# Kernel tuning notes

Hardware: AMD Instinct MI355X
Metric: run time of the kernel (lower is better)

Reference implementation:

```python
import jax, jax.numpy as jnp
import numpy as np

T, D, E, K = 16384, 2048, 64, 2
LOAD_BALANCE_SCALE = 0.01
NOISY_STD = 1.0


def setup_inputs() -> dict:
    key = jax.random.key(0)
    k1, k2, k3, k4 = jax.random.split(key, 4)
    x_flat = jax.random.normal(k1, (T, D), dtype=jnp.float32)
    noise = jax.random.normal(k2, (T, E), dtype=jnp.float32)
    # gate_linear: nn.Linear(D, E, bias=False) -> weight [E, D]
    W_gate = jax.random.normal(k3, (E, D), dtype=jnp.float32) * (1.0 / np.sqrt(D))
    # noise_weight initialized to zeros in torch; use small values so the
    # noisy path is exercised numerically.
    noise_weight = jax.random.normal(k4, (E,), dtype=jnp.float32) * 0.01
    return {"x_flat": x_flat, "noise": noise, "W_gate": W_gate,
            "noise_weight": noise_weight, "k": K}


def reference(x_flat, noise, W_gate, noise_weight, k):
    # logits = x @ W^T   [T, E]
    logits = jnp.einsum("td,ed->te", x_flat, W_gate)
    logits_noisy = logits + (noise * NOISY_STD) * noise_weight

    # noisy top-k; softmax over -inf-sparse logits == softmax over the k
    # selected logits scattered into zeros (top-k ids are unique per row).
    top_vals, top_ids = jax.lax.top_k(logits_noisy, k)          # [T, k]
    gates_k = jax.nn.softmax(top_vals, axis=-1)                 # [T, k]
    rows = jnp.arange(x_flat.shape[0])[:, None]
    top_k_gated_weights = jnp.zeros_like(logits_noisy).at[rows, top_ids].set(gates_k)

    # load-balance loss on clean logits
    gate_weights_mean = jax.nn.softmax(logits, axis=-1).mean(axis=0)  # [E]
    uniform = jnp.full_like(gate_weights_mean, 1.0 / gate_weights_mean.shape[0])
    load_balance_loss = jnp.mean((gate_weights_mean - uniform) ** 2) * LOAD_BALANCE_SCALE

    return top_k_gated_weights, top_ids, load_balance_loss
```

## Files before the change

### kernel.cpp

```cpp
#include <hip/hip_runtime.h>
#include <hip/hip_bf16.h>

#define T_TOK 16384
#define D_DIM 2048
#define E_EXP 64
#define TAU   2e-3f

typedef __bf16 bf16x8 __attribute__((ext_vector_type(8)));
typedef float  f32x16 __attribute__((ext_vector_type(16)));
typedef unsigned short ushort_t;

#define WS_WHI  0
#define WS_WLO  (256*1024)
#define WS_SUM  (512*1024)
#define WS_CNT  (512*1024 + 512)
#define WS_FLG  (512*1024 + 1024)

__device__ __forceinline__ unsigned short bf16_rne(float x){
  unsigned int u = __float_as_uint(x);
  return (unsigned short)((u + 0x7FFFu + ((u >> 16) & 1u)) >> 16);
}

__device__ __forceinline__ void ins3(float& v1, int& i1, float& v2, int& i2,
                                     float& v3, int& i3, float v, int i){
  if (v > v1 || (v == v1 && i < i1)) { v3=v2; i3=i2; v2=v1; i2=i1; v1=v; i1=i; }
  else if (v > v2 || (v == v2 && i < i2)) { v3=v2; i3=i2; v2=v; i2=i; }
  else if (v > v3 || (v == v3 && i < i3)) { v3=v; i3=i; }
}

__device__ __forceinline__ void gload16(const void* g, const void* l){
  __builtin_amdgcn_global_load_lds(
      (const __attribute__((address_space(1))) unsigned int*)g,
      (__attribute__((address_space(3))) unsigned int*)l, 16, 0, 0);
}

__global__ void wsplit_kernel(const float* __restrict__ W,
                              ushort_t* __restrict__ whi, ushort_t* __restrict__ wlo,
                              double* __restrict__ ESUM, int* __restrict__ FCNT){
  const int n = blockIdx.x * 256 + threadIdx.x;
  if (blockIdx.x == 0){
    if (threadIdx.x < 64) ESUM[threadIdx.x] = 0.0;
    else if (threadIdx.x == 64) *FCNT = 0;
  }
  const int e  = n >> 8;
  const int k0 = (n & 255) * 8;
  const float* src = W + (size_t)e*D_DIM + k0;
  float4 w0 = *reinterpret_cast<const float4*>(src);
  float4 w1 = *reinterpret_cast<const float4*>(src + 4);
  float f[8] = {w0.x,w0.y,w0.z,w0.w,w1.x,w1.y,w1.z,w1.w};
  unsigned h[8], lo[8];
  #pragma unroll
  for (int i = 0; i < 8; ++i){
    h[i]  = bf16_rne(f[i]);
    lo[i] = bf16_rne(f[i] - __uint_as_float(h[i] << 16));
  }
  uint4 hv = { h[0]|(h[1]<<16),  h[2]|(h[3]<<16),  h[4]|(h[5]<<16),  h[6]|(h[7]<<16) };
  uint4 lv = { lo[0]|(lo[1]<<16), lo[2]|(lo[3]<<16), lo[4]|(lo[5]<<16), lo[6]|(lo[7]<<16) };
  const int c  = k0 >> 7, ks = (k0 >> 6) & 1, t = (k0 >> 4) & 3, kg = (k0 >> 3) & 1;
  const int gidx = c*1024 + ks*512 + t*128 + (e >> 5)*64 + kg*32 + (e & 31);
  *reinterpret_cast<uint4*>(whi + (size_t)gidx*8) = hv;
  *reinterpret_cast<uint4*>(wlo + (size_t)gidx*8) = lv;
}

__launch_bounds__(512, 1)
__global__ void moe_main(const float* __restrict__ X, const float* __restrict__ NZ,
                         const ushort_t* __restrict__ WHI, const ushort_t* __restrict__ WLO,
                         const float* __restrict__ NW, float* __restrict__ OUT,
                         double* __restrict__ ESUM, int* __restrict__ FCNT,
                         int* __restrict__ FLIST)
{
  __shared__ __align__(16) char smem[65792];

  const int tid  = threadIdx.x;
  const int lane = tid & 63;
  const int wv   = tid >> 6;
  const int eh   = wv & 1;
  const int ks   = (wv >> 1) & 1;
  const int mh   = wv >> 2;
  const int r0   = blockIdx.x << 6;
  const int m    = lane & 31;
  const int kg   = lane >> 5;
  const int row  = mh*32 + m;

  const char* pq[4];
  #pragma unroll
  for (int q = 0; q < 4; ++q){
    const int rw = wv*8 + q*2 + (lane >> 5);
    const int gp = lane & 31;
    const int g  = (gp & 24) | ((gp ^ rw) & 7);
    pq[q] = (const char*)X + ((size_t)(r0 + rw)*D_DIM + g*4) * 4;
  }
  const char* pq0 = pq[0]; const char* pq1 = pq[1];
  const char* pq2 = pq[2]; const char* pq3 = pq[3];

  const char* pwh = (const char*)WHI + (size_t)(ks*512 + eh*64 + lane)*16;
  const char* pwl = (const char*)WLO + (size_t)(ks*512 + eh*64 + lane)*16;

  #define XOFF(t, h) (row*512 + ((((ks*16 + (t)*4 + kg*2 + (h)) & 24) | (((ks*16 + (t)*4 + kg*2 + (h)) ^ row) & 7)) << 4))
  const int xo00 = XOFF(0,0), xo01 = XOFF(0,1);
  const int xo10 = XOFF(1,0), xo11 = XOFF(1,1);
  const int xo20 = XOFF(2,0), xo21 = XOFF(2,1);
  const int xo30 = XOFF(3,0), xo31 = XOFF(3,1);
  #undef XOFF

  f32x16 acc;
  #pragma unroll
  for (int i = 0; i < 16; ++i) acc[i] = 0.0f;

  uint4 hA0,lA0,hA1,lA1,hA2,lA2,hA3,lA3;
  uint4 hB0,lB0,hB1,lB1,hB2,lB2,hB3,lB3;

  #define ISSUE(c, BUF, H0,L0,H1,L1,H2,L2,H3,L3) do{                           \
    __builtin_amdgcn_sched_barrier(0);                                         \
    gload16(pq0 + (size_t)(c)*512, smem + (BUF) + wv*4096);                    \
    gload16(pq1 + (size_t)(c)*512, smem + (BUF) + wv*4096 + 1024);             \
    gload16(pq2 + (size_t)(c)*512, smem + (BUF) + wv*4096 + 2048);             \
    gload16(pq3 + (size_t)(c)*512, smem + (BUF) + wv*4096 + 3072);             \
    H0 = *reinterpret_cast<const uint4*>(pwh + (size_t)(c)*16384);             \
    L0 = *reinterpret_cast<const uint4*>(pwl + (size_t)(c)*16384);             \
    H1 = *reinterpret_cast<const uint4*>(pwh + (size_t)(c)*16384 + 2048);      \
    L1 = *reinterpret_cast<const uint4*>(pwl + (size_t)(c)*16384 + 2048);      \
    H2 = *reinterpret_cast<const uint4*>(pwh + (size_t)(c)*16384 + 4096);      \
    L2 = *reinterpret_cast<const uint4*>(pwl + (size_t)(c)*16384 + 4096);      \
    H3 = *reinterpret_cast<const uint4*>(pwh + (size_t)(c)*16384 + 6144);      \
    L3 = *reinterpret_cast<const uint4*>(pwl + (size_t)(c)*16384 + 6144);      \
    __builtin_amdgcn_sched_barrier(0);                                         \
  }while(0)

  #define KSTEP(BUF, OA, OB, WH, WL) do{                                       \
    float4 fa = *reinterpret_cast<const float4*>(smem + (BUF) + (OA));         \
    float4 fb = *reinterpret_cast<const float4*>(smem + (BUF) + (OB));         \
    bf16x8 ah, al;                                                             \
    { float fv[8] = {fa.x,fa.y,fa.z,fa.w,fb.x,fb.y,fb.z,fb.w};                 \
      _Pragma("unroll")                                                        \
      for (int ii = 0; ii < 8; ++ii){                                          \
        __bf16 hh = (__bf16)fv[ii];                                            \
        ah[ii] = hh; al[ii] = (__bf16)(fv[ii] - (float)hh);                    \
      } }                                                                      \
    bf16x8 bh = __builtin_bit_cast(bf16x8, WH);                                \
    bf16x8 bl = __builtin_bit_cast(bf16x8, WL);                                \
    acc = __builtin_amdgcn_mfma_f32_32x32x16_bf16(ah, bh, acc, 0, 0, 0);       \
    acc = __builtin_amdgcn_mfma_f32_32x32x16_bf16(ah, bl, acc, 0, 0, 0);       \
    acc = __builtin_amdgcn_mfma_f32_32x32x16_bf16(al, bh, acc, 0, 0, 0);       \
  }while(0)

  #define COMPUTE(BUF, H0,L0,H1,L1,H2,L2,H3,L3) do{                            \
    KSTEP(BUF, xo00, xo01, H0, L0);                                            \
    KSTEP(BUF, xo10, xo11, H1, L1);                                            \
    KSTEP(BUF, xo20, xo21, H2, L2);                                            \
    KSTEP(BUF, xo30, xo31, H3, L3);                                            \
  }while(0)

  #define WAITV(N) do{ asm volatile("s_waitcnt vmcnt(" #N ")" ::: "memory");   \
                       __builtin_amdgcn_sched_barrier(0); }while(0)

  ISSUE(0, 0,     hA0,lA0,hA1,lA1,hA2,lA2,hA3,lA3);
  ISSUE(1, 32768, hB0,lB0,hB1,lB1,hB2,lB2,hB3,lB3);

  #pragma unroll 1
  for (int g = 0; g < 7; ++g){
    const int c = 2*g;
    WAITV(12); __builtin_amdgcn_s_barrier();
    COMPUTE(0, hA0,lA0,hA1,lA1,hA2,lA2,hA3,lA3);
    __builtin_amdgcn_s_barrier();
    ISSUE(c+2, 0, hA0,lA0,hA1,lA1,hA2,lA2,hA3,lA3);
    WAITV(12); __builtin_amdgcn_s_barrier();
    COMPUTE(32768, hB0,lB0,hB1,lB1,hB2,lB2,hB3,lB3);
    __builtin_amdgcn_s_barrier();
    ISSUE(c+3, 32768, hB0,lB0,hB1,lB1,hB2,lB2,hB3,lB3);
  }
  WAITV(12); __builtin_amdgcn_s_barrier();
  COMPUTE(0, hA0,lA0,hA1,lA1,hA2,lA2,hA3,lA3);
  __builtin_amdgcn_s_barrier();
  WAITV(0);  __builtin_amdgcn_s_barrier();
  COMPUTE(32768, hB0,lB0,hB1,lB1,hB2,lB2,hB3,lB3);

  #undef ISSUE
  #undef KSTEP
  #undef COMPUTE
  #undef WAITV

  float* lgts = (float*)(smem);
  float* nzs  = (float*)(smem + 16384);
  float* prb  = (float*)(smem + 32768);
  float* red  = (float*)(smem + 49152);
  float* nws  = (float*)(smem + 65536);
  const int ex = eh*32 + m;

  __syncthreads();
  if (ks == 1){
    #pragma unroll
    for (int r = 0; r < 16; ++r){
      int rr = (r & 3) + ((r >> 2) << 3) + (kg << 2);
      red[(mh*32 + rr)*64 + ex] = acc[r];
    }
  }
  __syncthreads();
  if (ks == 0){
    #pragma unroll
    for (int r = 0; r < 16; ++r){
      int rr = (r & 3) + ((r >> 2) << 3) + (kg << 2);
      int idx = (mh*32 + rr)*64 + ex;
      lgts[idx] = acc[r] + red[idx];
    }
  }
  {
    const int rw = tid >> 3, cb = (tid & 7) * 8;
    *reinterpret_cast<float4*>(&nzs[rw*64 + cb]) =
      *reinterpret_cast<const float4*>(NZ + (size_t)(r0 + rw)*E_EXP + cb);
    *reinterpret_cast<float4*>(&nzs[rw*64 + cb + 4]) =
      *reinterpret_cast<const float4*>(NZ + (size_t)(r0 + rw)*E_EXP + cb + 4);
  }
  if (tid < 64) nws[tid] = NW[tid];
  __syncthreads();

  {
    const int rrow = (wv << 3) + (lane >> 3);
    const int j    = lane & 7;
    const int trow = r0 + rrow;
    float cl[8];
    float v1 = -INFINITY, v2 = -INFINITY, v3 = -INFINITY;
    int   i1 = 1 << 29,   i2 = 1 << 29,   i3 = 1 << 29;
    #pragma unroll
    for (int mm = 0; mm < 8; ++mm){
      int q = j + (mm << 3);
      float lg = lgts[rrow*64 + q];
      cl[mm] = lg;
      float vn = fmaf(nzs[rrow*64 + q], nws[q], lg);
      ins3(v1,i1,v2,i2,v3,i3, vn, q);
    }
    #pragma unroll
    for (int d = 1; d < 8; d <<= 1){
      float ov1 = __shfl_xor(v1, d, 8), ov2 = __shfl_xor(v2, d, 8), ov3 = __shfl_xor(v3, d, 8);
      int   oi1 = __shfl_xor(i1, d, 8), oi2 = __shfl_xor(i2, d, 8), oi3 = __shfl_xor(i3, d, 8);
      ins3(v1,i1,v2,i2,v3,i3, ov1, oi1);
      ins3(v1,i1,v2,i2,v3,i3, ov2, oi2);
      ins3(v1,i1,v2,i2,v3,i3, ov3, oi3);
    }
    float e1 = expf(v2 - v1);
    float g0g = 1.0f / (1.0f + e1);
    float g1g = e1 * g0g;

    float mx = cl[0];
    #pragma unroll
    for (int mm = 1; mm < 8; ++mm) mx = fmaxf(mx, cl[mm]);
    #pragma unroll
    for (int d = 1; d < 8; d <<= 1) mx = fmaxf(mx, __shfl_xor(mx, d, 8));
    float sum = 0.0f, exv[8];
    #pragma unroll
    for (int mm = 0; mm < 8; ++mm){ exv[mm] = expf(cl[mm] - mx); sum += exv[mm]; }
    #pragma unroll
    for (int d = 1; d < 8; d <<= 1) sum += __shfl_xor(sum, d, 8);
    float inv = 1.0f / sum;
    #pragma unroll
    for (int mm = 0; mm < 8; ++mm) prb[rrow*64 + j + (mm << 3)] = exv[mm] * inv;

    if (j == 0){
      OUT[(size_t)T_TOK*E_EXP + (size_t)trow*2]     = (float)i1;
      OUT[(size_t)T_TOK*E_EXP + (size_t)trow*2 + 1] = (float)i2;
      if ((v1 - v2 < TAU) || (v2 - v3 < TAU)){
        int slot = atomicAdd(FCNT, 1);
        FLIST[slot] = trow;
      }
    }
    #pragma unroll
    for (int mm = 0; mm < 8; ++mm){
      int q = j + (mm << 3);
      lgts[rrow*64 + q] = (q == i1) ? g0g : ((q == i2) ? g1g : 0.0f);
    }
  }
  __syncthreads();

  {
    const int rw = tid >> 3, cb = (tid & 7) * 8;
    *reinterpret_cast<float4*>(OUT + (size_t)(r0 + rw)*E_EXP + cb) =
      *reinterpret_cast<const float4*>(&lgts[rw*64 + cb]);
    *reinterpret_cast<float4*>(OUT + (size_t)(r0 + rw)*E_EXP + cb + 4) =
      *reinterpret_cast<const float4*>(&lgts[rw*64 + cb + 4]);
  }
  if (tid < 64){
    float s0 = 0.0f;
    #pragma unroll 8
    for (int rr2 = 0; rr2 < 64; ++rr2) s0 += prb[rr2*64 + tid];
    atomicAdd(&ESUM[tid], (double)s0);
  }
}

__launch_bounds__(256)
__global__ void moe_fixup(const float* __restrict__ X, const float* __restrict__ NZ,
                          const float* __restrict__ WG, const float* __restrict__ NW,
                          float* __restrict__ OUT, const int* __restrict__ FCNT,
                          const int* __restrict__ FLIST)
{
  __shared__ __align__(16) float xl[2048];
  __shared__ double lz[64];
  __shared__ int   si1, si2;
  __shared__ float sg0, sg1;
  const int n    = *FCNT;
  const int lane = threadIdx.x & 63;
  const int wv   = threadIdx.x >> 6;
  for (int idx = blockIdx.x; idx < n; idx += gridDim.x){
    const int t = FLIST[idx];
    {
      int off = threadIdx.x * 8;
      *reinterpret_cast<float4*>(xl + off) =
        *reinterpret_cast<const float4*>(X + (size_t)t*D_DIM + off);
      *reinterpret_cast<float4*>(xl + off + 4) =
        *reinterpret_cast<const float4*>(X + (size_t)t*D_DIM + off + 4);
    }
    __syncthreads();
    for (int s = 0; s < 16; ++s){
      const int e = wv*16 + s;
      const float* wr = WG + (size_t)e*D_DIM;
      double acc = 0.0;
      #pragma unroll
      for (int it = 0; it < 8; ++it){
        float4 w4 = *reinterpret_cast<const float4*>(wr + it*256 + lane*4);
        float4 x4 = *reinterpret_cast<const float4*>(xl + it*256 + lane*4);
        acc += (double)x4.x * (double)w4.x;
        acc += (double)x4.y * (double)w4.y;
        acc += (double)x4.z * (double)w4.z;
        acc += (double)x4.w * (double)w4.w;
      }
      #pragma unroll
      for (int off = 1; off < 64; off <<= 1) acc += __shfl_xor(acc, off, 64);
      if (lane == 0)
        lz[e] = acc + (double)NZ[(size_t)t*E_EXP + e] * (double)NW[e];
    }
    __syncthreads();
    if (threadIdx.x == 0){
      double b1 = -1e300, b2 = -1e300; int j1 = 0, j2 = 0;
      for (int q = 0; q < 64; ++q){
        double v = lz[q];
        if (v > b1){ b2 = b1; j2 = j1; b1 = v; j1 = q; }
        else if (v > b2){ b2 = v; j2 = q; }
      }
      double ee = exp(b2 - b1);
      sg0 = (float)(1.0 / (1.0 + ee));
      sg1 = (float)(ee / (1.0 + ee));
      si1 = j1; si2 = j2;
      OUT[(size_t)T_TOK*E_EXP + (size_t)t*2]     = (float)j1;
      OUT[(size_t)T_TOK*E_EXP + (size_t)t*2 + 1] = (float)j2;
    }
    __syncthreads();
    if (threadIdx.x < 64)
      OUT[(size_t)t*E_EXP + threadIdx.x] = (threadIdx.x == si1) ? sg0 :
                                           ((threadIdx.x == si2) ? sg1 : 0.0f);
    __syncthreads();
  }
}

__global__ void moe_loss(const double* __restrict__ ESUM, float* __restrict__ OUT){
  const int e = threadIdx.x;
  double d = ESUM[e] * (1.0 / T_TOK) - (1.0 / 64.0);
  double sq = d * d;
  #pragma unroll
  for (int off = 1; off < 64; off <<= 1) sq += __shfl_xor(sq, off, 64);
  if (e == 0) OUT[(size_t)T_TOK*E_EXP + T_TOK*2] = (float)(sq * (0.01 / 64.0));
}

extern "C" void kernel_launch(void* const* d_in, const int* in_sizes, int n_in,
                              void* d_out, int out_size, void* d_ws, size_t ws_size,
                              hipStream_t stream)
{
  const float* X  = (const float*)d_in[0];
  const float* NZ = (const float*)d_in[1];
  const float* WG = (const float*)d_in[2];
  const float* NW = (const float*)d_in[3];
  float* OUT = (float*)d_out;
  char*  ws  = (char*)d_ws;
  ushort_t* WHI = (ushort_t*)(ws + WS_WHI);
  ushort_t* WLO = (ushort_t*)(ws + WS_WLO);
  double* ESUM = (double*)(ws + WS_SUM);
  int* FCNT  = (int*)(ws + WS_CNT);
  int* FLIST = (int*)(ws + WS_FLG);

  wsplit_kernel<<<dim3(64), dim3(256), 0, stream>>>(WG, WHI, WLO, ESUM, FCNT);
  moe_main<<<dim3(T_TOK/64), dim3(512), 0, stream>>>(X, NZ, WHI, WLO, NW, OUT, ESUM, FCNT, FLIST);
  moe_fixup<<<dim3(512), dim3(256), 0, stream>>>(X, NZ, WG, NW, OUT, FCNT, FLIST);
  moe_loss<<<dim3(1), dim3(64), 0, stream>>>(ESUM, OUT);
}
```

Baseline: 105.6 us.

## Keep W high-part in registers, stage W low-part in LDS with triple buffering

Rewrites the GEMM main loop so each wave splits K eight ways and computes a full 64x64 tile with four accumulators. The bf16 high half of its W slice is preloaded once into 32 registers, and only X and the low half of W are streamed through LDS. Buffering goes from two stages to three, and the weight-split kernel writes a simple linear layout to match. The aim is to cut redundant per-chunk W global loads and hide more latency, at the cost of a larger LDS footprint, more register pressure, and a wider cross-wave reduction.

Measured after the change: 102.7 us. 2.7% less time.

```diff
diff --git a/kernel.cpp b/kernel.cpp
--- a/kernel.cpp
+++ b/kernel.cpp
@@ -42,9 +42,12 @@
     if (threadIdx.x < 64) ESUM[threadIdx.x] = 0.0;
     else if (threadIdx.x == 64) *FCNT = 0;
   }
-  const int e  = n >> 8;
-  const int k0 = (n & 255) * 8;
-  const float* src = W + (size_t)e*D_DIM + k0;
+  const int lane = n & 63;
+  const int e    = (n >> 6) & 1;
+  const int w    = (n >> 7) & 7;
+  const int c    = n >> 10;
+  const float* src = W + (size_t)(e*32 + (lane & 31))*D_DIM
+                       + c*128 + w*16 + (lane >> 5)*8;
   float4 w0 = *reinterpret_cast<const float4*>(src);
   float4 w1 = *reinterpret_cast<const float4*>(src + 4);
   float f[8] = {w0.x,w0.y,w0.z,w0.w,w1.x,w1.y,w1.z,w1.w};
@@ -56,10 +59,8 @@
   }
   uint4 hv = { h[0]|(h[1]<<16),  h[2]|(h[3]<<16),  h[4]|(h[5]<<16),  h[6]|(h[7]<<16) };
   uint4 lv = { lo[0]|(lo[1]<<16), lo[2]|(lo[3]<<16), lo[4]|(lo[5]<<16), lo[6]|(lo[7]<<16) };
-  const int c  = k0 >> 7, ks = (k0 >> 6) & 1, t = (k0 >> 4) & 3, kg = (k0 >> 3) & 1;
-  const int gidx = c*1024 + ks*512 + t*128 + (e >> 5)*64 + kg*32 + (e & 31);
-  *reinterpret_cast<uint4*>(whi + (size_t)gidx*8) = hv;
-  *reinterpret_cast<uint4*>(wlo + (size_t)gidx*8) = lv;
+  *reinterpret_cast<uint4*>(whi + (size_t)n*8) = hv;
+  *reinterpret_cast<uint4*>(wlo + (size_t)n*8) = lv;
 }
 
 __launch_bounds__(512, 1)
@@ -69,141 +70,158 @@
                          double* __restrict__ ESUM, int* __restrict__ FCNT,
                          int* __restrict__ FLIST)
 {
-  __shared__ __align__(16) char smem[65792];
+  __shared__ __align__(16) char smem[147456];
 
   const int tid  = threadIdx.x;
   const int lane = tid & 63;
   const int wv   = tid >> 6;
-  const int eh   = wv & 1;
-  const int ks   = (wv >> 1) & 1;
-  const int mh   = wv >> 2;
   const int r0   = blockIdx.x << 6;
   const int m    = lane & 31;
   const int kg   = lane >> 5;
-  const int row  = mh*32 + m;
-
-  const char* pq[4];
+
+  const char *pq0, *pq1, *pq2, *pq3;
+  {
+    const char* p[4];
+    #pragma unroll
+    for (int q = 0; q < 4; ++q){
+      const int rw = wv*8 + q*2 + (lane >> 5);
+      const int gp = lane & 31;
+      const int g  = (gp & 24) | ((gp ^ rw) & 7);
+      p[q] = (const char*)X + ((size_t)(r0 + rw)*D_DIM + g*4) * 4;
+    }
+    pq0 = p[0]; pq1 = p[1]; pq2 = p[2]; pq3 = p[3];
+  }
+  const char* pwh = (const char*)WHI + wv*2048 + lane*16;
+  const char* pwl = (const char*)WLO + wv*2048 + lane*16;
+
+  const int g0  = wv*4 + kg*2;
+  const int xo0 = m*512 + (((g0  ) & 24) | (((g0  ) ^ m) & 7))*16;
+  const int xo1 = m*512 + (((g0+1) & 24) | (((g0+1) ^ m) & 7))*16;
+  const int wloo = 32768 + wv*2048 + lane*16;
+
+  f32x16 a00, a01, a10, a11;
   #pragma unroll
-  for (int q = 0; q < 4; ++q){
-    const int rw = wv*8 + q*2 + (lane >> 5);
-    const int gp = lane & 31;
-    const int g  = (gp & 24) | ((gp ^ rw) & 7);
-    pq[q] = (const char*)X + ((size_t)(r0 + rw)*D_DIM + g*4) * 4;
-  }
-  const char* pq0 = pq[0]; const char* pq1 = pq[1];
-  const char* pq2 = pq[2]; const char* pq3 = pq[3];
-
-  const char* pwh = (const char*)WHI + (size_t)(ks*512 + eh*64 + lane)*16;
-  const char* pwl = (const char*)WLO + (size_t)(ks*512 + eh*64 + lane)*16;
-
-  #define XOFF(t, h) (row*512 + ((((ks*16 + (t)*4 + kg*2 + (h)) & 24) | (((ks*16 + (t)*4 + kg*2 + (h)) ^ row) & 7)) << 4))
-  const int xo00 = XOFF(0,0), xo01 = XOFF(0,1);
-  const int xo10 = XOFF(1,0), xo11 = XOFF(1,1);
-  const int xo20 = XOFF(2,0), xo21 = XOFF(2,1);
-  const int xo30 = XOFF(3,0), xo31 = XOFF(3,1);
-  #undef XOFF
-
-  f32x16 acc;
+  for (int i = 0; i < 16; ++i){ a00[i]=0.f; a01[i]=0.f; a10[i]=0.f; a11[i]=0.f; }
+
+  uint4 wreg[32];
   #pragma unroll
-  for (int i = 0; i < 16; ++i) acc[i] = 0.0f;
-
-  uint4 hA0,lA0,hA1,lA1,hA2,lA2,hA3,lA3;
-  uint4 hB0,lB0,hB1,lB1,hB2,lB2,hB3,lB3;
-
-  #define ISSUE(c, BUF, H0,L0,H1,L1,H2,L2,H3,L3) do{                           \
+  for (int c2 = 0; c2 < 32; ++c2)
+    wreg[c2] = *reinterpret_cast<const uint4*>(pwh + (c2 >> 1)*16384 + (c2 & 1)*1024);
+
+  #define ISSUE(C, BUF) do{                                                    \
     __builtin_amdgcn_sched_barrier(0);                                         \
-    gload16(pq0 + (size_t)(c)*512, smem + (BUF) + wv*4096);                    \
-    gload16(pq1 + (size_t)(c)*512, smem + (BUF) + wv*4096 + 1024);             \
-    gload16(pq2 + (size_t)(c)*512, smem + (BUF) + wv*4096 + 2048);             \
-    gload16(pq3 + (size_t)(c)*512, smem + (BUF) + wv*4096 + 3072);             \
-    H0 = *reinterpret_cast<const uint4*>(pwh + (size_t)(c)*16384);             \
-    L0 = *reinterpret_cast<const uint4*>(pwl + (size_t)(c)*16384);             \
-    H1 = *reinterpret_cast<const uint4*>(pwh + (size_t)(c)*16384 + 2048);      \
-    L1 = *reinterpret_cast<const uint4*>(pwl + (size_t)(c)*16384 + 2048);      \
-    H2 = *reinterpret_cast<const uint4*>(pwh + (size_t)(c)*16384 + 4096);      \
-    L2 = *reinterpret_cast<const uint4*>(pwl + (size_t)(c)*16384 + 4096);      \
-    H3 = *reinterpret_cast<const uint4*>(pwh + (size_t)(c)*16384 + 6144);      \
-    L3 = *reinterpret_cast<const uint4*>(pwl + (size_t)(c)*16384 + 6144);      \
+    gload16(pq0 + (size_t)(C)*512, smem + (BUF) + wv*4096);                    \
+    gload16(pq1 + (size_t)(C)*512, smem + (BUF) + wv*4096 + 1024);             \
+    gload16(pq2 + (size_t)(C)*512, smem + (BUF) + wv*4096 + 2048);             \
+    gload16(pq3 + (size_t)(C)*512, smem + (BUF) + wv*4096 + 3072);             \
+    gload16(pwl + (size_t)(C)*16384,        smem + (BUF) + 32768 + wv*2048);         \
+    gload16(pwl + (size_t)(C)*16384 + 1024, smem + (BUF) + 32768 + wv*2048 + 1024);  \
     __builtin_amdgcn_sched_barrier(0);                                         \
   }while(0)
 
-  #define KSTEP(BUF, OA, OB, WH, WL) do{                                       \
-    float4 fa = *reinterpret_cast<const float4*>(smem + (BUF) + (OA));         \
-    float4 fb = *reinterpret_cast<const float4*>(smem + (BUF) + (OB));         \
-    bf16x8 ah, al;                                                             \
-    { float fv[8] = {fa.x,fa.y,fa.z,fa.w,fb.x,fb.y,fb.z,fb.w};                 \
+  #define COMPUTE(C, BUF) do{                                                  \
+    const char* Bx = smem + (BUF);                                             \
+    float4 fa0 = *reinterpret_cast<const float4*>(Bx + xo0);                   \
+    float4 fb0 = *reinterpret_cast<const float4*>(Bx + xo1);                   \
+    float4 fa1 = *reinterpret_cast<const float4*>(Bx + 16384 + xo0);           \
+    float4 fb1 = *reinterpret_cast<const float4*>(Bx + 16384 + xo1);           \
+    bf16x8 bl0 = *reinterpret_cast<const bf16x8*>(Bx + wloo);                  \
+    bf16x8 bl1 = *reinterpret_cast<const bf16x8*>(Bx + wloo + 1024);           \
+    bf16x8 ah0, al0, ah1, al1;                                                 \
+    { float fv[8] = {fa0.x,fa0.y,fa0.z,fa0.w,fb0.x,fb0.y,fb0.z,fb0.w};         \
       _Pragma("unroll")                                                        \
       for (int ii = 0; ii < 8; ++ii){                                          \
         __bf16 hh = (__bf16)fv[ii];                                            \
-        ah[ii] = hh; al[ii] = (__bf16)(fv[ii] - (float)hh);                    \
-      } }                                                                      \
-    bf16x8 bh = __builtin_bit_cast(bf16x8, WH);                                \
-    bf16x8 bl = __builtin_bit_cast(bf16x8, WL);                                \
-    acc = __builtin_amdgcn_mfma_f32_32x32x16_bf16(ah, bh, acc, 0, 0, 0);       \
-    acc = __builtin_amdgcn_mfma_f32_32x32x16_bf16(ah, bl, acc, 0, 0, 0);       \
-    acc = __builtin_amdgcn_mfma_f32_32x32x16_bf16(al, bh, acc, 0, 0, 0);       \
-  }while(0)
-
-  #define COMPUTE(BUF, H0,L0,H1,L1,H2,L2,H3,L3) do{                            \
-    KSTEP(BUF, xo00, xo01, H0, L0);                                            \
-    KSTEP(BUF, xo10, xo11, H1, L1);                                            \
-    KSTEP(BUF, xo20, xo21, H2, L2);                                            \
-    KSTEP(BUF, xo30, xo31, H3, L3);                                            \
+        ah0[ii] = hh; al0[ii] = (__bf16)(fv[ii] - (float)hh); } }              \
+    { float fv[8] = {fa1.x,fa1.y,fa1.z,fa1.w,fb1.x,fb1.y,fb1.z,fb1.w};         \
+      _Pragma("unroll")                                                        \
+      for (int ii = 0; ii < 8; ++ii){                                          \
+        __bf16 hh = (__bf16)fv[ii];                                            \
+        ah1[ii] = hh; al1[ii] = (__bf16)(fv[ii] - (float)hh); } }              \
+    bf16x8 bh0 = __builtin_bit_cast(bf16x8, wreg[(C)*2]);                      \
+    bf16x8 bh1 = __builtin_bit_cast(bf16x8, wreg[(C)*2 + 1]);                  \
+    a00 = __builtin_amdgcn_mfma_f32_32x32x16_bf16(ah0, bh0, a00, 0, 0, 0);     \
+    a00 = __builtin_amdgcn_mfma_f32_32x32x16_bf16(al0, bh0, a00, 0, 0, 0);     \
+    a00 = __builtin_amdgcn_mfma_f32_32x32x16_bf16(ah0, bl0, a00, 0, 0, 0);     \
+    a01 = __builtin_amdgcn_mfma_f32_32x32x16_bf16(ah0, bh1, a01, 0, 0, 0);     \
+    a01 = __builtin_amdgcn_mfma_f32_32x32x16_bf16(al0, bh1, a01, 0, 0, 0);     \
+    a01 = __builtin_amdgcn_mfma_f32_32x32x16_bf16(ah0, bl1, a01, 0, 0, 0);     \
+    a10 = __builtin_amdgcn_mfma_f32_32x32x16_bf16(ah1, bh0, a10, 0, 0, 0);     \
+    a10 = __builtin_amdgcn_mfma_f32_32x32x16_bf16(al1, bh0, a10, 0, 0, 0);     \
+    a10 = __builtin_amdgcn_mfma_f32_32x32x16_bf16(ah1, bl0, a10, 0, 0, 0);     \
+    a11 = __builtin_amdgcn_mfma_f32_32x32x16_bf16(ah1, bh1, a11, 0, 0, 0);     \
+    a11 = __builtin_amdgcn_mfma_f32_32x32x16_bf16(al1, bh1, a11, 0, 0, 0);     \
+    a11 = __builtin_amdgcn_mfma_f32_32x32x16_bf16(ah1, bl1, a11, 0, 0, 0);     \
   }while(0)
 
   #define WAITV(N) do{ asm volatile("s_waitcnt vmcnt(" #N ")" ::: "memory");   \
                        __builtin_amdgcn_sched_barrier(0); }while(0)
 
-  ISSUE(0, 0,     hA0,lA0,hA1,lA1,hA2,lA2,hA3,lA3);
-  ISSUE(1, 32768, hB0,lB0,hB1,lB1,hB2,lB2,hB3,lB3);
-
-  #pragma unroll 1
-  for (int g = 0; g < 7; ++g){
-    const int c = 2*g;
-    WAITV(12); __builtin_amdgcn_s_barrier();
-    COMPUTE(0, hA0,lA0,hA1,lA1,hA2,lA2,hA3,lA3);
-    __builtin_amdgcn_s_barrier();
-    ISSUE(c+2, 0, hA0,lA0,hA1,lA1,hA2,lA2,hA3,lA3);
-    WAITV(12); __builtin_amdgcn_s_barrier();
-    COMPUTE(32768, hB0,lB0,hB1,lB1,hB2,lB2,hB3,lB3);
-    __builtin_amdgcn_s_barrier();
-    ISSUE(c+3, 32768, hB0,lB0,hB1,lB1,hB2,lB2,hB3,lB3);
-  }
-  WAITV(12); __builtin_amdgcn_s_barrier();
-  COMPUTE(0, hA0,lA0,hA1,lA1,hA2,lA2,hA3,lA3);
-  __builtin_amdgcn_s_barrier();
-  WAITV(0);  __builtin_amdgcn_s_barrier();
-  COMPUTE(32768, hB0,lB0,hB1,lB1,hB2,lB2,hB3,lB3);
-
+  #define PHASE(C, TOK, DOISS) do{                                             \
+    WAITV(TOK); __builtin_amdgcn_s_barrier();                                  \
+    COMPUTE(C, ((C) % 3) * 49152);                                             \
+    __builtin_amdgcn_s_barrier();                                              \
+    if (DOISS) ISSUE((C) + 3, ((C) % 3) * 49152);                              \
+  }while(0)
+
+  ISSUE(0, 0); ISSUE(1, 49152); ISSUE(2, 98304);
+  WAITV(18);
+
+  PHASE(0,  12, 1);  PHASE(1,  12, 1);  PHASE(2,  12, 1);  PHASE(3,  12, 1);
+  PHASE(4,  12, 1);  PHASE(5,  12, 1);  PHASE(6,  12, 1);  PHASE(7,  12, 1);
+  PHASE(8,  12, 1);  PHASE(9,  12, 1);  PHASE(10, 12, 1);  PHASE(11, 12, 1);
+  PHASE(12, 12, 1);  PHASE(13, 12, 0);  PHASE(14, 6,  0);  PHASE(15, 0,  0);
+
+  #undef PHASE
+  #undef WAITV
+  #undef COMPUTE
   #undef ISSUE
-  #undef KSTEP
-  #undef COMPUTE
-  #undef WAITV
-
-  float* lgts = (float*)(smem);
-  float* nzs  = (float*)(smem + 16384);
-  float* prb  = (float*)(smem + 32768);
-  float* red  = (float*)(smem + 49152);
-  float* nws  = (float*)(smem + 65536);
-  const int ex = eh*32 + m;
-
-  __syncthreads();
-  if (ks == 1){
+
+  float* redp = (float*)(smem + ((wv & 3) < 3 ? (wv & 3)*16384 : 49152));
+  __syncthreads();
+  if (wv < 4){
     #pragma unroll
     for (int r = 0; r < 16; ++r){
       int rr = (r & 3) + ((r >> 2) << 3) + (kg << 2);
-      red[(mh*32 + rr)*64 + ex] = acc[r];
-    }
-  }
-  __syncthreads();
-  if (ks == 0){
+      redp[rr*64 + m]            = a00[r];
+      redp[rr*64 + 32 + m]       = a01[r];
+      redp[(32 + rr)*64 + m]     = a10[r];
+      redp[(32 + rr)*64 + 32 + m]= a11[r];
+    }
+  }
+  __syncthreads();
+  if (wv >= 4){
     #pragma unroll
     for (int r = 0; r < 16; ++r){
       int rr = (r & 3) + ((r >> 2) << 3) + (kg << 2);
-      int idx = (mh*32 + rr)*64 + ex;
-      lgts[idx] = acc[r] + red[idx];
-    }
-  }
+      redp[rr*64 + m]             += a00[r];
+      redp[rr*64 + 32 + m]        += a01[r];
+      redp[(32 + rr)*64 + m]      += a10[r];
+      redp[(32 + rr)*64 + 32 + m] += a11[r];
+    }
+  }
+  __syncthreads();
+  float* lgts = (float*)(smem);
+  {
+    const float4* r1 = (const float4*)(smem + 16384);
+    const float4* r2 = (const float4*)(smem + 32768);
+    const float4* r3 = (const float4*)(smem + 49152);
+    float4* r0 = (float4*)(smem);
+    #pragma unroll
+    for (int i = 0; i < 2; ++i){
+      int idx = tid*2 + i;
+      float4 s = r0[idx];
+      float4 b = r1[idx], c = r2[idx], d = r3[idx];
+      s.x += b.x + c.x + d.x; s.y += b.y + c.y + d.y;
+      s.z += b.z + c.z + d.z; s.w += b.w + c.w + d.w;
+      r0[idx] = s;
+    }
+  }
+  __syncthreads();
+
+  float* nzs = (float*)(smem + 16384);
+  float* prb = (float*)(smem + 32768);
+  float* nws = (float*)(smem + 65536);
   {
     const int rw = tid >> 3, cb = (tid & 7) * 8;
     *reinterpret_cast<float4*>(&nzs[rw*64 + cb]) =
```

## Restructure gate GEMM to 16x16 MFMA tiles with per-wave K-halves

Applied to the files above, without the earlier changes.

Switches the gate GEMM from 32x32x16 MFMA, with waves split over expert halves and K-slices, to 16x16x32 MFMA. Each wave now owns 16 rows and all 64 experts over one K-half, and the weight layout is reworked to match. Each wave keeps a private LDS double buffer, so the block-wide barriers in the main loop go away and the reduction buffer is dropped. Launch bounds are raised to allow 2 blocks per CU. The trade-off is more weight registers per wave (32 uint4), which puts register pressure against the higher occupancy target.

After: 102.3 us. -3.1%, faster.

```diff
diff --git a/kernel.cpp b/kernel.cpp
--- a/kernel.cpp
+++ b/kernel.cpp
@@ -7,7 +7,7 @@
 #define TAU   2e-3f
 
 typedef __bf16 bf16x8 __attribute__((ext_vector_type(8)));
-typedef float  f32x16 __attribute__((ext_vector_type(16)));
+typedef float  f32x4  __attribute__((ext_vector_type(4)));
 typedef unsigned short ushort_t;
 
 #define WS_WHI  0
@@ -56,153 +56,155 @@
   }
   uint4 hv = { h[0]|(h[1]<<16),  h[2]|(h[3]<<16),  h[4]|(h[5]<<16),  h[6]|(h[7]<<16) };
   uint4 lv = { lo[0]|(lo[1]<<16), lo[2]|(lo[3]<<16), lo[4]|(lo[5]<<16), lo[6]|(lo[7]<<16) };
-  const int c  = k0 >> 7, ks = (k0 >> 6) & 1, t = (k0 >> 4) & 3, kg = (k0 >> 3) & 1;
-  const int gidx = c*1024 + ks*512 + t*128 + (e >> 5)*64 + kg*32 + (e & 31);
-  *reinterpret_cast<uint4*>(whi + (size_t)gidx*8) = hv;
-  *reinterpret_cast<uint4*>(wlo + (size_t)gidx*8) = lv;
-}
-
-__launch_bounds__(512, 1)
+  const int kh = k0 >> 10, c = (k0 >> 6) & 15, s = (k0 >> 5) & 1, kg = (k0 >> 3) & 3;
+  const int t  = e >> 4;
+  const int G  = ((kh*16 + c)*8 + s*4 + t)*64 + kg*16 + (e & 15);
+  *reinterpret_cast<uint4*>(whi + (size_t)G*8) = hv;
+  *reinterpret_cast<uint4*>(wlo + (size_t)G*8) = lv;
+}
+
+__launch_bounds__(512, 2)
 __global__ void moe_main(const float* __restrict__ X, const float* __restrict__ NZ,
                          const ushort_t* __restrict__ WHI, const ushort_t* __restrict__ WLO,
                          const float* __restrict__ NW, float* __restrict__ OUT,
                          double* __restrict__ ESUM, int* __restrict__ FCNT,
                          int* __restrict__ FLIST)
 {
-  __shared__ __align__(16) char smem[65792];
+  __shared__ __align__(16) char smem[65536];
 
   const int tid  = threadIdx.x;
   const int lane = tid & 63;
   const int wv   = tid >> 6;
-  const int eh   = wv & 1;
-  const int ks   = (wv >> 1) & 1;
-  const int mh   = wv >> 2;
+  const int kh   = wv & 1;
+  const int pair = wv >> 1;
   const int r0   = blockIdx.x << 6;
-  const int m    = lane & 31;
-  const int kg   = lane >> 5;
-  const int row  = mh*32 + m;
-
-  const char* pq[4];
+  const int pr0  = r0 + pair*16;
+
+  char* ldsbase = smem + wv*8192;
+
+  const char *px0, *px1, *px2, *px3;
+  {
+    const char* p[4];
+    #pragma unroll
+    for (int q = 0; q < 4; ++q){
+      const int row = q*4 + (lane >> 4);
+      const int g   = (lane & 15) ^ row;
+      p[q] = (const char*)X + ((size_t)(pr0 + row)*D_DIM + kh*1024 + g*4) * 4;
+    }
+    px0 = p[0]; px1 = p[1]; px2 = p[2]; px3 = p[3];
+  }
+  const char* pwh = (const char*)WHI + (size_t)kh*131072 + lane*16;
+  const char* pwl = (const char*)WLO + (size_t)kh*131072 + lane*16;
+
+  const int arow = lane & 15, akg = lane >> 4;
+  const int xo00 = arow*256 + (((0*8 + akg*2 + 0) ^ arow) << 4);
+  const int xo01 = arow*256 + (((0*8 + akg*2 + 1) ^ arow) << 4);
+  const int xo10 = arow*256 + (((1*8 + akg*2 + 0) ^ arow) << 4);
+  const int xo11 = arow*256 + (((1*8 + akg*2 + 1) ^ arow) << 4);
+
+  f32x4 acc[4];
   #pragma unroll
-  for (int q = 0; q < 4; ++q){
-    const int rw = wv*8 + q*2 + (lane >> 5);
-    const int gp = lane & 31;
-    const int g  = (gp & 24) | ((gp ^ rw) & 7);
-    pq[q] = (const char*)X + ((size_t)(r0 + rw)*D_DIM + g*4) * 4;
-  }
-  const char* pq0 = pq[0]; const char* pq1 = pq[1];
-  const char* pq2 = pq[2]; const char* pq3 = pq[3];
-
-  const char* pwh = (const char*)WHI + (size_t)(ks*512 + eh*64 + lane)*16;
-  const char* pwl = (const char*)WLO + (size_t)(ks*512 + eh*64 + lane)*16;
-
-  #define XOFF(t, h) (row*512 + ((((ks*16 + (t)*4 + kg*2 + (h)) & 24) | (((ks*16 + (t)*4 + kg*2 + (h)) ^ row) & 7)) << 4))
-  const int xo00 = XOFF(0,0), xo01 = XOFF(0,1);
-  const int xo10 = XOFF(1,0), xo11 = XOFF(1,1);
-  const int xo20 = XOFF(2,0), xo21 = XOFF(2,1);
-  const int xo30 = XOFF(3,0), xo31 = XOFF(3,1);
-  #undef XOFF
-
-  f32x16 acc;
-  #pragma unroll
-  for (int i = 0; i < 16; ++i) acc[i] = 0.0f;
-
-  uint4 hA0,lA0,hA1,lA1,hA2,lA2,hA3,lA3;
-  uint4 hB0,lB0,hB1,lB1,hB2,lB2,hB3,lB3;
-
-  #define ISSUE(c, BUF, H0,L0,H1,L1,H2,L2,H3,L3) do{                           \
+  for (int t = 0; t < 4; ++t){ acc[t][0]=0.f; acc[t][1]=0.f; acc[t][2]=0.f; acc[t][3]=0.f; }
+
+  uint4 wAh[8], wAl[8], wBh[8], wBl[8];
+
+  #define LOADX(C, BUF) do{                                                    \
     __builtin_amdgcn_sched_barrier(0);                                         \
-    gload16(pq0 + (size_t)(c)*512, smem + (BUF) + wv*4096);                    \
-    gload16(pq1 + (size_t)(c)*512, smem + (BUF) + wv*4096 + 1024);             \
-    gload16(pq2 + (size_t)(c)*512, smem + (BUF) + wv*4096 + 2048);             \
-    gload16(pq3 + (size_t)(c)*512, smem + (BUF) + wv*4096 + 3072);             \
-    H0 = *reinterpret_cast<const uint4*>(pwh + (size_t)(c)*16384);             \
-    L0 = *reinterpret_cast<const uint4*>(pwl + (size_t)(c)*16384);             \
-    H1 = *reinterpret_cast<const uint4*>(pwh + (size_t)(c)*16384 + 2048);      \
-    L1 = *reinterpret_cast<const uint4*>(pwl + (size_t)(c)*16384 + 2048);      \
-    H2 = *reinterpret_cast<const uint4*>(pwh + (size_t)(c)*16384 + 4096);      \
-    L2 = *reinterpret_cast<const uint4*>(pwl + (size_t)(c)*16384 + 4096);      \
-    H3 = *reinterpret_cast<const uint4*>(pwh + (size_t)(c)*16384 + 6144);      \
-    L3 = *reinterpret_cast<const uint4*>(pwl + (size_t)(c)*16384 + 6144);      \
+    gload16(px0 + (size_t)(C)*256, ldsbase + (BUF)*4096);                      \
+    gload16(px1 + (size_t)(C)*256, ldsbase + (BUF)*4096 + 1024);               \
+    gload16(px2 + (size_t)(C)*256, ldsbase + (BUF)*4096 + 2048);               \
+    gload16(px3 + (size_t)(C)*256, ldsbase + (BUF)*4096 + 3072);               \
     __builtin_amdgcn_sched_barrier(0);                                         \
   }while(0)
 
-  #define KSTEP(BUF, OA, OB, WH, WL) do{                                       \
-    float4 fa = *reinterpret_cast<const float4*>(smem + (BUF) + (OA));         \
-    float4 fb = *reinterpret_cast<const float4*>(smem + (BUF) + (OB));         \
-    bf16x8 ah, al;                                                             \
-    { float fv[8] = {fa.x,fa.y,fa.z,fa.w,fb.x,fb.y,fb.z,fb.w};                 \
+  #define LOADW(C, WH, WL) do{                                                 \
+    _Pragma("unroll")                                                          \
+    for (int i = 0; i < 8; ++i){                                               \
+      WH[i] = *reinterpret_cast<const uint4*>(pwh + (size_t)(C)*8192 + i*1024);\
+      WL[i] = *reinterpret_cast<const uint4*>(pwl + (size_t)(C)*8192 + i*1024);\
+    }                                                                          \
+  }while(0)
+
+  #define CVT8(fa, fb, ah, al) do{                                             \
+    float fv[8] = {fa.x,fa.y,fa.z,fa.w,fb.x,fb.y,fb.z,fb.w};                   \
+    _Pragma("unroll")                                                          \
+    for (int ii = 0; ii < 8; ++ii){                                            \
+      __bf16 hh = (__bf16)fv[ii];                                              \
+      ah[ii] = hh; al[ii] = (__bf16)(fv[ii] - (float)hh);                      \
+    }                                                                          \
+  }while(0)
+
+  #define COMPUTE(BUF, WH, WL) do{                                             \
+    const char* Bx = ldsbase + (BUF)*4096;                                     \
+    { float4 fa = *reinterpret_cast<const float4*>(Bx + xo00);                 \
+      float4 fb = *reinterpret_cast<const float4*>(Bx + xo01);                 \
+      bf16x8 ah, al; CVT8(fa, fb, ah, al);                                     \
       _Pragma("unroll")                                                        \
-      for (int ii = 0; ii < 8; ++ii){                                          \
-        __bf16 hh = (__bf16)fv[ii];                                            \
-        ah[ii] = hh; al[ii] = (__bf16)(fv[ii] - (float)hh);                    \
+      for (int t = 0; t < 4; ++t){                                             \
+        bf16x8 bh = __builtin_bit_cast(bf16x8, WH[t]);                         \
+        bf16x8 bl = __builtin_bit_cast(bf16x8, WL[t]);                         \
+        acc[t] = __builtin_amdgcn_mfma_f32_16x16x32_bf16(ah, bh, acc[t],0,0,0);\
+        acc[t] = __builtin_amdgcn_mfma_f32_16x16x32_bf16(al, bh, acc[t],0,0,0);\
+        acc[t] = __builtin_amdgcn_mfma_f32_16x16x32_bf16(ah, bl, acc[t],0,0,0);\
       } }                                                                      \
-    bf16x8 bh = __builtin_bit_cast(bf16x8, WH);                                \
-    bf16x8 bl = __builtin_bit_cast(bf16x8, WL);                                \
-    acc = __builtin_amdgcn_mfma_f32_32x32x16_bf16(ah, bh, acc, 0, 0, 0);       \
-    acc = __builtin_amdgcn_mfma_f32_32x32x16_bf16(ah, bl, acc, 0, 0, 0);       \
-    acc = __builtin_amdgcn_mfma_f32_32x32x16_bf16(al, bh, acc, 0, 0, 0);       \
+    { float4 fa = *reinterpret_cast<const float4*>(Bx + xo10);                 \
+      float4 fb = *reinterpret_cast<const float4*>(Bx + xo11);                 \
+      bf16x8 ah, al; CVT8(fa, fb, ah, al);                                     \
+      _Pragma("unroll")                                                        \
+      for (int t = 0; t < 4; ++t){                                             \
+        bf16x8 bh = __builtin_bit_cast(bf16x8, WH[4+t]);                       \
+        bf16x8 bl = __builtin_bit_cast(bf16x8, WL[4+t]);                       \
+        acc[t] = __builtin_amdgcn_mfma_f32_16x16x32_bf16(ah, bh, acc[t],0,0,0);\
+        acc[t] = __builtin_amdgcn_mfma_f32_16x16x32_bf16(al, bh, acc[t],0,0,0);\
+        acc[t] = __builtin_amdgcn_mfma_f32_16x16x32_bf16(ah, bl, acc[t],0,0,0);\
+      } }                                                                      \
   }while(0)
 
-  #define COMPUTE(BUF, H0,L0,H1,L1,H2,L2,H3,L3) do{                            \
-    KSTEP(BUF, xo00, xo01, H0, L0);                                            \
-    KSTEP(BUF, xo10, xo11, H1, L1);                                            \
-    KSTEP(BUF, xo20, xo21, H2, L2);                                            \
-    KSTEP(BUF, xo30, xo31, H3, L3);                                            \
-  }while(0)
-
-  #define WAITV(N) do{ asm volatile("s_waitcnt vmcnt(" #N ")" ::: "memory");   \
+  #define WAITX(N) do{ asm volatile("s_waitcnt vmcnt(" #N ")" ::: "memory");   \
                        __builtin_amdgcn_sched_barrier(0); }while(0)
 
-  ISSUE(0, 0,     hA0,lA0,hA1,lA1,hA2,lA2,hA3,lA3);
-  ISSUE(1, 32768, hB0,lB0,hB1,lB1,hB2,lB2,hB3,lB3);
+  LOADX(0, 0); LOADW(0, wAh, wAl);
+  LOADX(1, 1); LOADW(1, wBh, wBl);
 
   #pragma unroll 1
   for (int g = 0; g < 7; ++g){
     const int c = 2*g;
-    WAITV(12); __builtin_amdgcn_s_barrier();
-    COMPUTE(0, hA0,lA0,hA1,lA1,hA2,lA2,hA3,lA3);
-    __builtin_amdgcn_s_barrier();
-    ISSUE(c+2, 0, hA0,lA0,hA1,lA1,hA2,lA2,hA3,lA3);
-    WAITV(12); __builtin_amdgcn_s_barrier();
-    COMPUTE(32768, hB0,lB0,hB1,lB1,hB2,lB2,hB3,lB3);
-    __builtin_amdgcn_s_barrier();
-    ISSUE(c+3, 32768, hB0,lB0,hB1,lB1,hB2,lB2,hB3,lB3);
-  }
-  WAITV(12); __builtin_amdgcn_s_barrier();
-  COMPUTE(0, hA0,lA0,hA1,lA1,hA2,lA2,hA3,lA3);
-  __builtin_amdgcn_s_barrier();
-  WAITV(0);  __builtin_amdgcn_s_barrier();
-  COMPUTE(32768, hB0,lB0,hB1,lB1,hB2,lB2,hB3,lB3);
-
-  #undef ISSUE
-  #undef KSTEP
+    WAITX(20);
+    COMPUTE(0, wAh, wAl);
+    LOADX(c+2, 0); LOADW(c+2, wAh, wAl);
+    WAITX(20);
+    COMPUTE(1, wBh, wBl);
+    LOADX(c+3, 1); LOADW(c+3, wBh, wBl);
+  }
+  WAITX(20); COMPUTE(0, wAh, wAl);
+  WAITX(0);  COMPUTE(1, wBh, wBl);
+
+  #undef WAITX
   #undef COMPUTE
-  #undef WAITV
+  #undef CVT8
+  #undef LOADW
+  #undef LOADX
 
   float* lgts = (float*)(smem);
   float* nzs  = (float*)(smem + 16384);
   float* prb  = (float*)(smem + 32768);
-  float* red  = (float*)(smem + 49152);
-  float* nws  = (float*)(smem + 65536);
-  const int ex = eh*32 + m;
+  float* nws  = (float*)(smem + 49152);
 
   __syncthreads();
-  if (ks == 1){
-    #pragma unroll
-    for (int r = 0; r < 16; ++r){
-      int rr = (r & 3) + ((r >> 2) << 3) + (kg << 2);
-      red[(mh*32 + rr)*64 + ex] = acc[r];
-    }
+  if (kh == 0){
+    #pragma unroll
+    for (int t = 0; t < 4; ++t)
+      #pragma unroll
+      for (int r = 0; r < 4; ++r)
+        lgts[(pair*16 + akg*4 + r)*64 + t*16 + arow] = acc[t][r];
   }
   __syncthreads();
-  if (ks == 0){
-    #pragma unroll
-    for (int r = 0; r < 16; ++r){
-      int rr = (r & 3) + ((r >> 2) << 3) + (kg << 2);
-      int idx = (mh*32 + rr)*64 + ex;
-      lgts[idx] = acc[r] + red[idx];
-    }
+  if (kh == 1){
+    #pragma unroll
+    for (int t = 0; t < 4; ++t)
+      #pragma unroll
+      for (int r = 0; r < 4; ++r)
+        lgts[(pair*16 + akg*4 + r)*64 + t*16 + arow] += acc[t][r];
   }
   {
     const int rw = tid >> 3, cb = (tid & 7) * 8;
```
